# Kernel tuning notes

Hardware: AMD Instinct MI355X
Metric: run time of the kernel (lower is better)

## Reference

```python
import math
import jax, jax.numpy as jnp
import numpy as np

# Module config (init_kwargs)
GRID = (11, 16, 24)          # (T, H, W) latent grid, T odd so T-1 == 2*(T//2)
POOL = 128                   # pool_size / block size
SPARSITY = 0.9
TXT_LEN = 384                # txt_len, txt_first=False
HEADS, HDIM = 8, 128
FFL = GRID[1] * GRID[2]      # first_frame_len = H*W = 384
SEQ = GRID[0] * FFL + TXT_LEN  # 4608 tokens, 36 blocks of 128


def _rearr(t):
    # rearrange_with_remaining, h%8==0 and w%8==0 path.
    # t: [b, (f h w), n, d] with f = T-1 frames (first frame excluded)
    b, s, n, d = t.shape
    T, H, W = GRID
    fn, hn, wn = T // 2, H // 8, W // 8
    x = t.transpose(0, 2, 1, 3).reshape(b * n, fn, 2, hn, 8, wn, 8, d)
    # 'b (fn fb)(hn hb)(wn wb) d -> b (fn hn wn fb hb wb) d'
    x = x.transpose(0, 1, 3, 5, 2, 4, 6, 7).reshape(b * n, s, d)
    return x.reshape(b, n, s, d).transpose(0, 2, 1, 3)


def _inv_rearr(t):
    b, s, n, d = t.shape
    T, H, W = GRID
    fn, hn, wn = T // 2, H // 8, W // 8
    x = t.transpose(0, 2, 1, 3).reshape(b * n, fn, hn, wn, 2, 8, 8, d)
    x = x.transpose(0, 1, 4, 2, 5, 3, 6, 7).reshape(b * n, s, d)
    return x.reshape(b, n, s, d).transpose(0, 2, 1, 3)


def _avgpool(t):
    # seq divisible by POOL -> mean over each block (tail branch unused)
    b, s, n, d = t.shape
    return t.reshape(b, s // POOL, POOL, n, d).mean(axis=2)


def _forward(q, k, v):
    b, s, n, d = q.shape
    scale = jnp.asarray(d, q.dtype) ** -0.5
    # do_tensor_rearrange_pooling on concatenated qkv (txt_first=False)
    qkv = jnp.concatenate([q, k, v], axis=0)
    f_part = qkv[:, :FFL]
    i_part = qkv[:, FFL:s - TXT_LEN]
    t_part = qkv[:, s - TXT_LEN:]
    qkv2 = jnp.concatenate([_rearr(i_part), f_part, t_part], axis=1)
    pool = _avgpool(qkv2)
    q2, k2, v2 = jnp.split(qkv2, 3, axis=0)
    qp, kp, _ = jnp.split(pool, 3, axis=0)
    # pooled block scores + softmax
    ps = jax.nn.softmax(jnp.einsum('blnd,bsnd->bnls', qp, kp) * scale, axis=-1)
    nb = s // POOL
    keep = math.ceil(nb * (1.0 - SPARSITY))
    thr = jax.lax.top_k(ps, keep)[0][..., -1:]
    mask = ps >= thr                              # [B, n, nb, nb] bool
    prot = (FFL + TXT_LEN + POOL - 1) // POOL
    mask = mask.at[:, :, -prot:, :].set(True)
    mask = mask.at[:, :, :, -prot:].set(True)
    bm = mask[0]                                  # [n, nb, nb] per-head block mask (batch 0, as kernel uses)
    tok = jnp.repeat(jnp.repeat(bm, POOL, axis=1), POOL, axis=2)  # [n, S, S]
    # block-sparse attention == masked dense attention over selected kv blocks
    scores = jnp.einsum('bqnd,bknd->bnqk', q2, k2) * scale
    scores = jnp.where(tok[None], scores, jnp.asarray(-1e30, scores.dtype))
    p = jax.nn.softmax(scores, axis=-1)
    x = jnp.einsum('bnqk,bknd->bqnd', p, v2)
    # do_tensor_inv_rearrange (txt_first=False: concat(f, i, t))
    si = s - TXT_LEN - FFL
    xi = _inv_rearr(x[:, :si])
    xf = x[:, si:si + FFL]
    xt = x[:, si + FFL:]
    return jnp.concatenate([xf, xi, xt], axis=1)


def setup_inputs() -> dict:
    key = jax.random.key(0)
    kq, kk, kv = jax.random.split(key, 3)
    q = jax.random.normal(kq, (1, SEQ, HEADS, HDIM), dtype=jnp.float32)
    k = jax.random.normal(kk, (1, SEQ, HEADS, HDIM), dtype=jnp.float32)
    v = jax.random.normal(kv, (1, SEQ, HEADS, HDIM), dtype=jnp.float32)
    t_b_idx = jnp.arange(2, dtype=jnp.int64 if jax.config.jax_enable_x64 else jnp.int32)
    return {'q': q, 'k': k, 'v': v, 't_b_idx': t_b_idx}


def reference(q, k, v, t_b_idx):
    # t_idx = t_b_idx[0] = 0, skip_timesteps = 0 -> sparse branch (static)
    return _forward(q, k, v)
```

## Files before the change

### kernel.cpp

```cpp
#include <hip/hip_runtime.h>


typedef __attribute__((ext_vector_type(8))) _Float16 half8;
typedef __attribute__((ext_vector_type(4))) _Float16 half4;
typedef __attribute__((ext_vector_type(4))) float float4v;

#define KROW 136
#define VROW 72
#define PROW 72

__device__ __forceinline__ int orig_pos(int j) {
    if (j >= 3840) return (j < 4224) ? (j - 3840) : j;
    int blk = j >> 7;
    int r   = j & 127;
    int f   = blk / 6;
    int rem = blk - f * 6;
    int b2  = rem / 3;
    int e   = rem - b2 * 3;
    int a   = r >> 6;
    int c   = (r >> 3) & 7;
    int g   = r & 7;
    return 384 + (f * 2 + a) * 384 + (b2 * 8 + c) * 24 + e * 8 + g;
}

__device__ __forceinline__ void cp16(const void* g, void* l) {
    __builtin_amdgcn_global_load_lds((const __attribute__((address_space(1))) void*)g,
                                     (__attribute__((address_space(3))) void*)l, 16, 0, 0);
}

__global__ __launch_bounds__(256) void prep_kernel(const float* __restrict__ q,
                                                   const float* __restrict__ k,
                                                   const float* __restrict__ v,
                                                   short* __restrict__ Kc,
                                                   unsigned* __restrict__ Vt32,
                                                   float* __restrict__ qp,
                                                   float* __restrict__ kp) {
    __shared__ short Vs[64 * KROW];
    __shared__ float Rs[8 * 128];
    int bx  = blockIdx.x;
    int tid = threadIdx.x;
    int sub = bx & 1;
    int kb  = (bx >> 1) % 36;
    int h   = bx / 72;

    {
        int lt  = tid >> 2;
        int tok = sub * 64 + lt;
        int d0  = (tid & 3) << 5;
        int op  = orig_pos(kb * 128 + tok);
        const float* kr = k + ((size_t)op * 8 + h) * 128 + d0;
        const float* vr = v + ((size_t)op * 8 + h) * 128 + d0;
        short* ko = Kc + ((size_t)(h * 36 + kb) * 128 + tok) * KROW + d0;
#pragma unroll
        for (int j = 0; j < 32; j += 4) {
            float4v xk = *reinterpret_cast<const float4v*>(kr + j);
            float4v xv = *reinterpret_cast<const float4v*>(vr + j);
            half4 hk, hv;
#pragma unroll
            for (int i = 0; i < 4; ++i) { hk[i] = (_Float16)xk[i]; hv[i] = (_Float16)xv[i]; }
            *reinterpret_cast<half4*>(ko + j) = hk;
            *reinterpret_cast<half4*>(&Vs[lt * KROW + d0 + j]) = hv;
        }
    }

    {
        const float* arr = sub ? q : k;
        int dq = (tid & 31) << 2;
        int g  = tid >> 5;
        float4v acc = {0.f, 0.f, 0.f, 0.f};
        for (int t = g; t < 128; t += 8) {
            int op = orig_pos(kb * 128 + t);
            float4v x = *reinterpret_cast<const float4v*>(arr + ((size_t)op * 8 + h) * 128 + dq);
            acc[0] += x[0]; acc[1] += x[1]; acc[2] += x[2]; acc[3] += x[3];
        }
#pragma unroll
        for (int i = 0; i < 4; ++i) Rs[g * 128 + dq + i] = acc[i];
    }
    __syncthreads();

    {
        const unsigned short* Vsu = (const unsigned short*)Vs;
        unsigned* vo = Vt32 + (size_t)((h * 36 + kb) * 2 + sub) * 128 * (VROW / 2);
#pragma unroll
        for (int it = 0; it < 16; ++it) {
            int i   = it * 256 + tid;
            int tw  = i & 31;
            int dim = i >> 5;
            unsigned lo = Vsu[(2 * tw) * KROW + dim];
            unsigned hi = Vsu[(2 * tw + 1) * KROW + dim];
            vo[dim * (VROW / 2) + tw] = (hi << 16) | lo;
        }
    }

    if (tid < 128) {
        float s = 0.f;
#pragma unroll
        for (int g = 0; g < 8; ++g) s += Rs[g * 128 + tid];
        float* outp = sub ? qp : kp;
        outp[(h * 36 + kb) * 128 + tid] = s * (1.f / 128.f);
    }
}

__global__ void select_kernel(const float* __restrict__ qp, const float* __restrict__ kp,
                              int* __restrict__ lists) {
    int qb = blockIdx.x % 36;
    int h  = blockIdx.x / 36;
    int lane = threadIdx.x;
    float s = -1e30f;
    if (lane < 36) {
        const float4v* qv = (const float4v*)(qp + (h * 36 + qb) * 128);
        const float4v* kv = (const float4v*)(kp + (h * 36 + lane) * 128);
        float acc = 0.f;
        for (int i = 0; i < 32; ++i) {
            float4v a = qv[i], b = kv[i];
            acc += a[0] * b[0] + a[1] * b[1] + a[2] * b[2] + a[3] * b[3];
        }
        s = acc;
    }
    float tmp = s;
    float thr = 0.f;
    for (int i = 0; i < 4; ++i) {
        float mx = tmp;
        for (int off = 1; off < 64; off <<= 1) mx = fmaxf(mx, __shfl_xor(mx, off));
        thr = mx;
        unsigned long long bal = __ballot(tmp == mx);
        int low = __ffsll(bal) - 1;
        if (lane == low) tmp = -3e38f;
    }
    bool keep = (lane < 36) && ((s >= thr) || (qb >= 30) || (lane >= 30));
    unsigned long long mk = __ballot(keep);
    int* L = lists + (h * 36 + qb) * 40;
    if (lane == 0) L[0] = __popcll(mk);
    if (keep) {
        int pos = __popcll(mk & ((1ull << lane) - 1ull));
        L[1 + pos] = lane;
    }
}

__global__ __launch_bounds__(256, 3) void flash_kernel(const float* __restrict__ q,
                                                       const short* __restrict__ Kc,
                                                       const short* __restrict__ Vt,
                                                       const int* __restrict__ lists,
                                                       float* __restrict__ out,
                                                       float* __restrict__ pO,
                                                       float* __restrict__ pL) {
    __shared__ __align__(16) short Ks[64 * KROW];
    __shared__ __align__(16) short Vsh[128 * VROW];
    __shared__ __align__(16) short Ph[4 * 16 * PROW];

    int t = blockIdx.x;
    int h, qb, half, nkb = 0, kbase = 0, pidx = -1;
    if (t < 288) {
        h = t / 36;
        int r = t % 36;
        int qbh = r / 6, r2 = r % 6;
        half = r2 / 3;
        int chunk = r2 % 3;
        qb = 30 + qbh; nkb = 12; kbase = chunk * 12; pidx = t;
    } else {
        int t2 = t - 288;
        h = t2 / 60;
        int rem = t2 % 60;
        qb = rem >> 1; half = rem & 1;
    }
    const int* L = lists + (h * 36 + qb) * 40;
    if (pidx < 0) nkb = L[0];

    int tid = threadIdx.x, wave = tid >> 6, lane = tid & 63;
    int m16 = lane & 15, quad = lane >> 4;

    int qrow_frag = qb * 128 + half * 64 + wave * 16 + m16;
    const float* qrp = q + ((size_t)orig_pos(qrow_frag) * 8 + h) * 128;
    half8 aq[4];
#pragma unroll
    for (int kc = 0; kc < 4; ++kc) {
        float4v x0 = *reinterpret_cast<const float4v*>(qrp + kc * 32 + quad * 8);
        float4v x1 = *reinterpret_cast<const float4v*>(qrp + kc * 32 + quad * 8 + 4);
#pragma unroll
        for (int j = 0; j < 4; ++j) { aq[kc][j] = (_Float16)x0[j]; aq[kc][4 + j] = (_Float16)x1[j]; }
    }

    float l_r[4], o[8][4];
#pragma unroll
    for (int r = 0; r < 4; ++r) l_r[r] = 0.f;
#pragma unroll
    for (int dt = 0; dt < 8; ++dt)
#pragma unroll
        for (int r = 0; r < 4; ++r) o[dt][r] = 0.f;

    constexpr float kScale = 0.08838834764831845f * 1.4426950408889634f;
    short* Phw = Ph + wave * (16 * PROW);

    int ntile = nkb * 2;
    for (int it = 0; it < ntile; ++it) {
        int kb  = (pidx >= 0) ? (kbase + (it >> 1)) : L[1 + (it >> 1)];
        int sub = it & 1;
        const char* gK = (const char*)(Kc + ((size_t)((h * 36 + kb) * 128) + sub * 64) * KROW);
        const char* gV = (const char*)(Vt + (size_t)((h * 36 + kb) * 2 + sub) * 128 * VROW);

        __syncthreads();
        {
            char* lK = (char*)Ks;
            char* lV = (char*)Vsh;
            int off = lane * 16;
            for (int c = wave; c < 35; c += 4) {
                if (c < 17) cp16(gK + c * 1024 + off, lK + c * 1024 + off);
                else        cp16(gV + (c - 17) * 1024 + off, lV + (c - 17) * 1024 + off);
            }
        }
        __syncthreads();

        float4v sacc[4];
#pragma unroll
        for (int nt = 0; nt < 4; ++nt) { sacc[nt][0] = 0.f; sacc[nt][1] = 0.f; sacc[nt][2] = 0.f; sacc[nt][3] = 0.f; }
#pragma unroll
        for (int nt = 0; nt < 4; ++nt)
#pragma unroll
            for (int kc = 0; kc < 4; ++kc) {
                half8 bk = *reinterpret_cast<const half8*>(&Ks[(nt * 16 + m16) * KROW + kc * 32 + quad * 8]);
                sacc[nt] = __builtin_amdgcn_mfma_f32_16x16x32_f16(aq[kc], bk, sacc[nt], 0, 0, 0);
            }

#pragma unroll
        for (int r = 0; r < 4; ++r) {
            float p0 = exp2f(sacc[0][r] * kScale);
            float p1 = exp2f(sacc[1][r] * kScale);
            float p2 = exp2f(sacc[2][r] * kScale);
            float p3 = exp2f(sacc[3][r] * kScale);
            sacc[0][r] = p0; sacc[1][r] = p1; sacc[2][r] = p2; sacc[3][r] = p3;
            l_r[r] += (p0 + p1) + (p2 + p3);
        }

#pragma unroll
        for (int nt = 0; nt < 4; ++nt)
#pragma unroll
            for (int r = 0; r < 4; ++r) {
                union { _Float16 hf; short s; } cv;
                cv.hf = (_Float16)sacc[nt][r];
                Phw[(quad * 4 + r) * PROW + nt * 16 + m16] = cv.s;
            }
        half8 ap0 = *reinterpret_cast<const half8*>(&Phw[m16 * PROW + quad * 8]);
        half8 ap1 = *reinterpret_cast<const half8*>(&Phw[m16 * PROW + 32 + quad * 8]);

#pragma unroll
        for (int dt = 0; dt < 8; ++dt) {
            float4v oc;
            oc[0] = o[dt][0]; oc[1] = o[dt][1]; oc[2] = o[dt][2]; oc[3] = o[dt][3];
            half8 bv0 = *reinterpret_cast<const half8*>(&Vsh[(dt * 16 + m16) * VROW + quad * 8]);
            half8 bv1 = *reinterpret_cast<const half8*>(&Vsh[(dt * 16 + m16) * VROW + 32 + quad * 8]);
            oc = __builtin_amdgcn_mfma_f32_16x16x32_f16(ap0, bv0, oc, 0, 0, 0);
            oc = __builtin_amdgcn_mfma_f32_16x16x32_f16(ap1, bv1, oc, 0, 0, 0);
            o[dt][0] = oc[0]; o[dt][1] = oc[1]; o[dt][2] = oc[2]; o[dt][3] = oc[3];
        }
    }

#pragma unroll
    for (int r = 0; r < 4; ++r)
        for (int sh = 1; sh < 16; sh <<= 1) l_r[r] += __shfl_xor(l_r[r], sh);

    if (pidx >= 0) {
        float* po = pO + (size_t)pidx * 8192;
#pragma unroll
        for (int r = 0; r < 4; ++r) {
            int row = wave * 16 + quad * 4 + r;
#pragma unroll
            for (int dt = 0; dt < 8; ++dt)
                po[row * 128 + dt * 16 + m16] = o[dt][r];
            if (m16 == 0) pL[pidx * 64 + row] = l_r[r];
        }
    } else {
#pragma unroll
        for (int r = 0; r < 4; ++r) {
            int qrow = qb * 128 + half * 64 + wave * 16 + quad * 4 + r;
            size_t base = ((size_t)orig_pos(qrow) * 8 + h) * 128;
            float inv = 1.f / l_r[r];
#pragma unroll
            for (int dt = 0; dt < 8; ++dt)
                out[base + dt * 16 + m16] = o[dt][r] * inv;
        }
    }
}

__global__ void combine_kernel(const float* __restrict__ pO, const float* __restrict__ pL,
                               float* __restrict__ out) {
    int g = blockIdx.x;
    int h    = g / 12;
    int rem  = g % 12;
    int qbh  = rem >> 1;
    int half = rem & 1;
    int qb   = 30 + qbh;
    int base_t = ((h * 6 + qbh) * 2 + half) * 3;

    int tid = threadIdx.x;
    int d   = tid & 127;
    int r0  = tid >> 7;
    for (int itr = 0; itr < 32; ++itr) {
        int row = r0 + itr * 2;
        float l = pL[(base_t + 0) * 64 + row] + pL[(base_t + 1) * 64 + row] + pL[(base_t + 2) * 64 + row];
        float acc = pO[(size_t)(base_t + 0) * 8192 + row * 128 + d]
                  + pO[(size_t)(base_t + 1) * 8192 + row * 128 + d]
                  + pO[(size_t)(base_t + 2) * 8192 + row * 128 + d];
        int qrow = qb * 128 + half * 64 + row;
        out[((size_t)orig_pos(qrow) * 8 + h) * 128 + d] = acc / l;
    }
}

extern "C" void kernel_launch(void* const* d_in, const int* in_sizes, int n_in,
                              void* d_out, int out_size, void* d_ws, size_t ws_size,
                              hipStream_t stream) {
    const float* q = (const float*)d_in[0];
    const float* k = (const float*)d_in[1];
    const float* v = (const float*)d_in[2];
    float* out = (float*)d_out;

    char* w = (char*)d_ws;
    short* Kc  = (short*)(w);
    short* Vt  = (short*)(w + 10027008);
    float* qp  = (float*)(w + 20643840);
    float* kp  = (float*)(w + 20791296);
    int*   lst = (int*)  (w + 20938752);
    float* pL  = (float*)(w + 20984832);
    float* pO  = (float*)(w + 21058560);

    prep_kernel<<<dim3(576), dim3(256), 0, stream>>>(q, k, v, Kc, (unsigned*)Vt, qp, kp);
    select_kernel<<<dim3(288), dim3(64), 0, stream>>>(qp, kp, lst);
    flash_kernel<<<dim3(768), dim3(256), 0, stream>>>(q, Kc, Vt, lst, out, pO, pL);
    combine_kernel<<<dim3(96), dim3(256), 0, stream>>>(pO, pL, out);
}
```

Measured before the change: 203.0 us.

## Fuse block selection into flash kernel and interleave heads across blocks

```diff
diff --git a/kernel.cpp b/kernel.cpp
--- a/kernel.cpp
+++ b/kernel.cpp
@@ -44,22 +44,27 @@
     int h   = bx / 72;
 
     {
-        int lt  = tid >> 2;
-        int tok = sub * 64 + lt;
-        int d0  = (tid & 3) << 5;
-        int op  = orig_pos(kb * 128 + tok);
-        const float* kr = k + ((size_t)op * 8 + h) * 128 + d0;
-        const float* vr = v + ((size_t)op * 8 + h) * 128 + d0;
-        short* ko = Kc + ((size_t)(h * 36 + kb) * 128 + tok) * KROW + d0;
-#pragma unroll
-        for (int j = 0; j < 32; j += 4) {
-            float4v xk = *reinterpret_cast<const float4v*>(kr + j);
-            float4v xv = *reinterpret_cast<const float4v*>(vr + j);
-            half4 hk, hv;
-#pragma unroll
-            for (int i = 0; i < 4; ++i) { hk[i] = (_Float16)xk[i]; hv[i] = (_Float16)xv[i]; }
-            *reinterpret_cast<half4*>(ko + j) = hk;
-            *reinterpret_cast<half4*>(&Vs[lt * KROW + d0 + j]) = hv;
+        int lr = tid >> 3;
+        int ld = (tid & 7) << 2;
+#pragma unroll
+        for (int pass = 0; pass < 2; ++pass) {
+            int lt  = pass * 32 + lr;
+            int tok = sub * 64 + lt;
+            int op  = orig_pos(kb * 128 + tok);
+            const float* kr = k + ((size_t)op * 8 + h) * 128;
+            const float* vr = v + ((size_t)op * 8 + h) * 128;
+            short* ko = Kc + ((size_t)(h * 36 + kb) * 128 + tok) * KROW;
+#pragma unroll
+            for (int j = 0; j < 4; ++j) {
+                int d = ld + j * 32;
+                float4v xk = *reinterpret_cast<const float4v*>(kr + d);
+                float4v xv = *reinterpret_cast<const float4v*>(vr + d);
+                half4 hk, hv;
+#pragma unroll
+                for (int i = 0; i < 4; ++i) { hk[i] = (_Float16)xk[i]; hv[i] = (_Float16)xv[i]; }
+                *reinterpret_cast<half4*>(ko + d) = hk;
+                *reinterpret_cast<half4*>(&Vs[lt * KROW + d]) = hv;
+            }
         }
     }
 
@@ -101,70 +106,34 @@
     }
 }
 
-__global__ void select_kernel(const float* __restrict__ qp, const float* __restrict__ kp,
-                              int* __restrict__ lists) {
-    int qb = blockIdx.x % 36;
-    int h  = blockIdx.x / 36;
-    int lane = threadIdx.x;
-    float s = -1e30f;
-    if (lane < 36) {
-        const float4v* qv = (const float4v*)(qp + (h * 36 + qb) * 128);
-        const float4v* kv = (const float4v*)(kp + (h * 36 + lane) * 128);
-        float acc = 0.f;
-        for (int i = 0; i < 32; ++i) {
-            float4v a = qv[i], b = kv[i];
-            acc += a[0] * b[0] + a[1] * b[1] + a[2] * b[2] + a[3] * b[3];
-        }
-        s = acc;
-    }
-    float tmp = s;
-    float thr = 0.f;
-    for (int i = 0; i < 4; ++i) {
-        float mx = tmp;
-        for (int off = 1; off < 64; off <<= 1) mx = fmaxf(mx, __shfl_xor(mx, off));
-        thr = mx;
-        unsigned long long bal = __ballot(tmp == mx);
-        int low = __ffsll(bal) - 1;
-        if (lane == low) tmp = -3e38f;
-    }
-    bool keep = (lane < 36) && ((s >= thr) || (qb >= 30) || (lane >= 30));
-    unsigned long long mk = __ballot(keep);
-    int* L = lists + (h * 36 + qb) * 40;
-    if (lane == 0) L[0] = __popcll(mk);
-    if (keep) {
-        int pos = __popcll(mk & ((1ull << lane) - 1ull));
-        L[1 + pos] = lane;
-    }
-}
-
 __global__ __launch_bounds__(256, 3) void flash_kernel(const float* __restrict__ q,
                                                        const short* __restrict__ Kc,
                                                        const short* __restrict__ Vt,
-                                                       const int* __restrict__ lists,
+                                                       const float* __restrict__ qp,
+                                                       const float* __restrict__ kp,
                                                        float* __restrict__ out,
                                                        float* __restrict__ pO,
                                                        float* __restrict__ pL) {
     __shared__ __align__(16) short Ks[64 * KROW];
     __shared__ __align__(16) short Vsh[128 * VROW];
     __shared__ __align__(16) short Ph[4 * 16 * PROW];
+    __shared__ int Ls[40];
 
     int t = blockIdx.x;
     int h, qb, half, nkb = 0, kbase = 0, pidx = -1;
     if (t < 288) {
-        h = t / 36;
-        int r = t % 36;
-        int qbh = r / 6, r2 = r % 6;
+        h = t & 7;
+        int rest = t >> 3;
+        int qbh = rest / 6, r2 = rest % 6;
         half = r2 / 3;
         int chunk = r2 % 3;
         qb = 30 + qbh; nkb = 12; kbase = chunk * 12; pidx = t;
     } else {
         int t2 = t - 288;
-        h = t2 / 60;
-        int rem = t2 % 60;
-        qb = rem >> 1; half = rem & 1;
-    }
-    const int* L = lists + (h * 36 + qb) * 40;
-    if (pidx < 0) nkb = L[0];
+        h = t2 & 7;
+        int rest = t2 >> 3;
+        qb = rest >> 1; half = rest & 1;
+    }
 
     int tid = threadIdx.x, wave = tid >> 6, lane = tid & 63;
     int m16 = lane & 15, quad = lane >> 4;
@@ -180,6 +149,39 @@
         for (int j = 0; j < 4; ++j) { aq[kc][j] = (_Float16)x0[j]; aq[kc][4 + j] = (_Float16)x1[j]; }
     }
 
+    if (pidx < 0 && wave == 0) {
+        float s = -1e30f;
+        if (lane < 36) {
+            const float4v* qv = (const float4v*)(qp + (h * 36 + qb) * 128);
+            const float4v* kv = (const float4v*)(kp + (h * 36 + lane) * 128);
+            float acc = 0.f;
+            for (int i = 0; i < 32; ++i) {
+                float4v a = qv[i], b = kv[i];
+                acc += a[0] * b[0] + a[1] * b[1] + a[2] * b[2] + a[3] * b[3];
+            }
+            s = acc;
+        }
+        float tmp = s;
+        float thr = 0.f;
+        for (int i = 0; i < 4; ++i) {
+            float mx = tmp;
+            for (int off = 1; off < 64; off <<= 1) mx = fmaxf(mx, __shfl_xor(mx, off));
+            thr = mx;
+            unsigned long long bal = __ballot(tmp == mx);
+            int low = __ffsll(bal) - 1;
+            if (lane == low) tmp = -3e38f;
+        }
+        bool keep = (lane < 36) && ((s >= thr) || (lane >= 30));
+        unsigned long long mk = __ballot(keep);
+        if (lane == 0) Ls[0] = __popcll(mk);
+        if (keep) {
+            int pos = __popcll(mk & ((1ull << lane) - 1ull));
+            Ls[1 + pos] = lane;
+        }
+    }
+    __syncthreads();
+    if (pidx < 0) nkb = Ls[0];
+
     float l_r[4], o[8][4];
 #pragma unroll
     for (int r = 0; r < 4; ++r) l_r[r] = 0.f;
@@ -193,7 +195,7 @@
 
     int ntile = nkb * 2;
     for (int it = 0; it < ntile; ++it) {
-        int kb  = (pidx >= 0) ? (kbase + (it >> 1)) : L[1 + (it >> 1)];
+        int kb  = (pidx >= 0) ? (kbase + (it >> 1)) : Ls[1 + (it >> 1)];
         int sub = it & 1;
         const char* gK = (const char*)(Kc + ((size_t)((h * 36 + kb) * 128) + sub * 64) * KROW);
         const char* gV = (const char*)(Vt + (size_t)((h * 36 + kb) * 2 + sub) * 128 * VROW);
@@ -289,17 +291,17 @@
     int qbh  = rem >> 1;
     int half = rem & 1;
     int qb   = 30 + qbh;
-    int base_t = ((h * 6 + qbh) * 2 + half) * 3;
+    int base_t = (qbh * 6 + half * 3) * 8 + h;
 
     int tid = threadIdx.x;
     int d   = tid & 127;
     int r0  = tid >> 7;
     for (int itr = 0; itr < 32; ++itr) {
         int row = r0 + itr * 2;
-        float l = pL[(base_t + 0) * 64 + row] + pL[(base_t + 1) * 64 + row] + pL[(base_t + 2) * 64 + row];
+        float l = pL[(base_t + 0) * 64 + row] + pL[(base_t + 8) * 64 + row] + pL[(base_t + 16) * 64 + row];
         float acc = pO[(size_t)(base_t + 0) * 8192 + row * 128 + d]
-                  + pO[(size_t)(base_t + 1) * 8192 + row * 128 + d]
-                  + pO[(size_t)(base_t + 2) * 8192 + row * 128 + d];
+                  + pO[(size_t)(base_t + 8) * 8192 + row * 128 + d]
+                  + pO[(size_t)(base_t + 16) * 8192 + row * 128 + d];
         int qrow = qb * 128 + half * 64 + row;
         out[((size_t)orig_pos(qrow) * 8 + h) * 128 + d] = acc / l;
     }
@@ -318,12 +320,10 @@
     short* Vt  = (short*)(w + 10027008);
     float* qp  = (float*)(w + 20643840);
     float* kp  = (float*)(w + 20791296);
-    int*   lst = (int*)  (w + 20938752);
-    float* pL  = (float*)(w + 20984832);
-    float* pO  = (float*)(w + 21058560);
+    float* pL  = (float*)(w + 20938752);
+    float* pO  = (float*)(w + 21012480);
 
     prep_kernel<<<dim3(576), dim3(256), 0, stream>>>(q, k, v, Kc, (unsigned*)Vt, qp, kp);
-    select_kernel<<<dim3(288), dim3(64), 0, stream>>>(qp, kp, lst);
-    flash_kernel<<<dim3(768), dim3(256), 0, stream>>>(q, Kc, Vt, lst, out, pO, pL);
+    flash_kernel<<<dim3(768), dim3(256), 0, stream>>>(q, Kc, Vt, qp, kp, out, pO, pL);
     combine_kernel<<<dim3(96), dim3(256), 0, stream>>>(pO, pL, out);
 }
```

Measured after the change: 191.2 us. 1.06x faster.
